# Kernel optimization log

Measured on AMD Instinct MI355X. Metric: run time of the kernel, lower is better.

Reference implementation:

```python
import jax, jax.numpy as jnp
import numpy as np

B, L, D = 4, 2048, 256
H, DH, MLP, MAX_REL = 8, 32, 1024, 16
LN_EPS = 1e-5


def _layernorm(x, g, b):
    mu = jnp.mean(x, axis=-1, keepdims=True)
    var = jnp.mean(jnp.square(x - mu), axis=-1, keepdims=True)
    return (x - mu) * jax.lax.rsqrt(var + LN_EPS) * g + b


def setup_inputs() -> dict:
    key = jax.random.key(0)
    ks = jax.random.split(key, 16)
    s = 0.02
    return {
        "x": jax.random.normal(ks[0], (B, L, D), jnp.float32),
        "key_padding_mask": jax.random.randint(ks[1], (B, L), 0, 2).astype(bool),
        "Wqkv": jax.random.normal(ks[2], (D, 3 * D), jnp.float32) * s,
        "bqkv": jnp.zeros((3 * D,), jnp.float32),
        "Wo": jax.random.normal(ks[3], (D, D), jnp.float32) * s,
        "bo": jnp.zeros((D,), jnp.float32),
        "ln1_g": jnp.ones((D,), jnp.float32),
        "ln1_b": jnp.zeros((D,), jnp.float32),
        "W1": jax.random.normal(ks[4], (D, MLP), jnp.float32) * s,
        "b1": jnp.zeros((MLP,), jnp.float32),
        "W2": jax.random.normal(ks[5], (MLP, D), jnp.float32) * s,
        "b2": jnp.zeros((D,), jnp.float32),
        "ln2_g": jnp.ones((D,), jnp.float32),
        "ln2_b": jnp.zeros((D,), jnp.float32),
        "rel_bias": jax.random.normal(ks[6], (2 * MAX_REL + 1, H), jnp.float32) * 0.01,
    }


def reference(x, key_padding_mask, Wqkv, bqkv, Wo, bo, ln1_g, ln1_b,
              W1, b1, W2, b2, ln2_g, ln2_b, rel_bias):
    Bx, Lw, Dm = x.shape
    scale = DH ** -0.5
    qkv = x @ Wqkv + bqkv                                   # [B,L,3D]
    q, k, v = jnp.split(qkv, 3, axis=-1)
    q = q.reshape(Bx, Lw, H, DH).transpose(0, 2, 1, 3)      # [B,H,L,dh]
    k = k.reshape(Bx, Lw, H, DH).transpose(0, 2, 1, 3)
    v = v.reshape(Bx, Lw, H, DH).transpose(0, 2, 1, 3)
    scores = jnp.einsum("bhqd,bhkd->bhqk", q, k) * scale    # [B,H,L,L]
    idx = jnp.arange(Lw)
    rel_clip = jnp.clip(idx[None, :] - idx[:, None], -MAX_REL, MAX_REL) + MAX_REL
    bias = rel_bias[rel_clip].transpose(2, 0, 1)            # [H,L,L]
    scores = scores + bias[None]
    scores = jnp.where(key_padding_mask[:, None, None, :], jnp.float32(-1e9), scores)
    attn = jax.nn.softmax(scores, axis=-1)                  # dropout = identity (eval)
    out = jnp.einsum("bhqk,bhkd->bhqd", attn, v)
    out = out.transpose(0, 2, 1, 3).reshape(Bx, Lw, Dm)
    out = out @ Wo + bo
    x = _layernorm(x + out, ln1_g, ln1_b)
    m = jax.nn.relu(x @ W1 + b1) @ W2 + b2
    x = _layernorm(x + m, ln2_g, ln2_b)
    return x
```

## Files before the change

kernel.cpp:

```cpp
#include <hip/hip_runtime.h>

#define B_   4
#define L_   2048
#define D_   256
#define H_   8
#define DH_  32
#define MLP_ 1024
#define LOG2E 1.4426950408889634f

typedef __attribute__((ext_vector_type(8))) short  short8;
typedef __attribute__((ext_vector_type(4))) float  f32x4;
typedef __attribute__((ext_vector_type(2))) float  f32x2;
typedef unsigned long long ull;

union FragU { short8 v; struct { ull lo, hi; } q; unsigned u[4]; };
union SU { f32x4 v4; f32x2 v2[2]; };

__device__ __forceinline__ unsigned short f2bf(float f) {
  unsigned u = __float_as_uint(f);
  u += 0x7fffu + ((u >> 16) & 1u);
  return (unsigned short)(u >> 16);
}

__device__ __forceinline__ ull pack4(float a, float b, float c, float d) {
  return (ull)f2bf(a) | ((ull)f2bf(b) << 16) | ((ull)f2bf(c) << 32) | ((ull)f2bf(d) << 48);
}

__device__ __forceinline__ unsigned cvt_pk_bf16(float lo, float hi) {
  unsigned r;
  asm("v_cvt_pk_bf16_f32 %0, %1, %2" : "=v"(r) : "v"(lo), "v"(hi));
  return r;
}

__device__ __forceinline__ f32x2 pk_add(f32x2 a, f32x2 b) {
  f32x2 r; asm("v_pk_add_f32 %0, %1, %2" : "=v"(r) : "v"(a), "v"(b)); return r;
}

__device__ __forceinline__ float fexp2(float x) {
#if __has_builtin(__builtin_amdgcn_exp2f)
  return __builtin_amdgcn_exp2f(x);
#else
  return exp2f(x);
#endif
}

#define GLL16(gp, lp) __builtin_amdgcn_global_load_lds( \
    (const __attribute__((address_space(1))) void*)(gp), \
    (__attribute__((address_space(3))) void*)(lp), 16, 0, 0)

__global__ void prep_w(const float* __restrict__ x,
                       const float* __restrict__ Wqkv, const float* __restrict__ Wo,
                       const float* __restrict__ W1, const float* __restrict__ W2,
                       const int* __restrict__ mask, const float* __restrict__ relb,
                       unsigned short* __restrict__ xb,
                       unsigned short* __restrict__ wqkvt, unsigned short* __restrict__ wot,
                       unsigned short* __restrict__ w1t, unsigned short* __restrict__ w2t,
                       float* __restrict__ maskf,
                       float* __restrict__ mlo, float* __restrict__ mhi) {
  const int i = blockIdx.x * 256 + threadIdx.x;
  if (i < 524288) {
    const float4 v = *(const float4*)(x + (size_t)i * 4);
    *(ull*)(xb + (size_t)i * 4) = pack4(v.x, v.y, v.z, v.w);
  } else if (i < 720896) {
    const int j = i - 524288, r = j / 768, c = j - r * 768;
    wqkvt[(size_t)c * 256 + r] = f2bf(Wqkv[j]);
  } else if (i < 786432) {
    const int j = i - 720896, r = j >> 8, c = j & 255;
    wot[(size_t)c * 256 + r] = f2bf(Wo[j]);
  } else if (i < 1048576) {
    const int j = i - 786432, r = j >> 10, c = j & 1023;
    w1t[(size_t)c * 256 + r] = f2bf(W1[j]);
  } else if (i < 1310720) {
    const int j = i - 1048576, r = j >> 8, c = j & 255;
    w2t[(size_t)c * 1024 + r] = f2bf(W2[j]);
  } else if (i < 1318912) {
    const int j = i - 1310720;
    maskf[j] = mask[j] ? -1e9f : 0.f;
  } else {
    const int j2 = i - 1318912;
    const int t = j2 >> 16, idx = j2 & 65535;
    const int bh = idx >> 11, j = idx & 2047;
    const int bq = bh >> 3, h = bh & 7;
    const float base = mask[bq * L_ + j] ? -1e9f : 0.f;
    const float bias = relb[(t ? 32 * H_ : 0) + h] * LOG2E;
    (t ? mhi : mlo)[idx] = base + bias;
  }
}

template <int MODE, int TM, int TN, int NBX, int BYG>
__launch_bounds__(256)
__global__ void gemm_k(const unsigned short* __restrict__ A,
                       const unsigned short* __restrict__ Bt,
                       const float* __restrict__ bias,
                       unsigned short* __restrict__ outb0,
                       unsigned short* __restrict__ outb1,
                       unsigned short* __restrict__ outb2,
                       int K)
{
  constexpr int MI = TM / 32, NI = TN / 32;
  __shared__ alignas(16) unsigned short As[2][TM * 64];
  __shared__ alignas(16) unsigned short Bs[2][TN * 64];
  const int tid  = threadIdx.x;
  const int lane = tid & 63, wv = tid >> 6;
  const int wr = wv >> 1, wc = wv & 1;
  const int lr = lane & 15, g = lane >> 4;
  const int bid = blockIdx.x;
  const int xcd = bid & 7, ii = bid >> 3;
  const int by = xcd * BYG + ii / NBX;
  const int bx = ii % NBX;
  const int m0 = by * TM, n0 = bx * TN;
  const int l8 = lane >> 3, jj = lane & 7;

  auto stage = [&](int buf, int k0) {
#pragma unroll
    for (int i = 0; i < MI; ++i) {
      const int row = i * 32 + wv * 8 + l8;
      GLL16(A + (size_t)(m0 + row) * K + k0 + ((jj ^ (row & 7)) * 8),
            &As[buf][i * 2048 + wv * 512]);
    }
#pragma unroll
    for (int i = 0; i < NI; ++i) {
      const int row = i * 32 + wv * 8 + l8;
      GLL16(Bt + (size_t)(n0 + row) * K + k0 + ((jj ^ (row & 7)) * 8),
            &Bs[buf][i * 2048 + wv * 512]);
    }
  };

  f32x4 acc[MI][NI];
#pragma unroll
  for (int i = 0; i < MI; ++i)
#pragma unroll
    for (int j = 0; j < NI; ++j) acc[i][j] = (f32x4)(0.f);

  stage(0, 0);
  for (int k0 = 0; k0 < K; k0 += 64) {
    const int cur = (k0 >> 6) & 1;
    if (k0 + 64 < K) {
      stage(cur ^ 1, k0 + 64);
      asm volatile("s_waitcnt vmcnt(%0)" :: "n"(MI + NI) : "memory");
    } else {
      asm volatile("s_waitcnt vmcnt(0)" ::: "memory");
    }
    __builtin_amdgcn_sched_barrier(0);
    __builtin_amdgcn_s_barrier();
#pragma unroll
    for (int kk = 0; kk < 2; ++kk) {
      FragU af[MI], bf[NI];
#pragma unroll
      for (int mi = 0; mi < MI; ++mi) {
        const int row = wr * (TM / 2) + mi * 16 + lr;
        const int sw = (row & 7) << 3;
        af[mi].q.lo = *(const ull*)&As[cur][row * 64 + ((kk * 32 + 4 * g) ^ sw)];
        af[mi].q.hi = *(const ull*)&As[cur][row * 64 + ((kk * 32 + 16 + 4 * g) ^ sw)];
      }
#pragma unroll
      for (int ni = 0; ni < NI; ++ni) {
        const int row = wc * (TN / 2) + ni * 16 + lr;
        const int sw = (row & 7) << 3;
        bf[ni].q.lo = *(const ull*)&Bs[cur][row * 64 + ((kk * 32 + 4 * g) ^ sw)];
        bf[ni].q.hi = *(const ull*)&Bs[cur][row * 64 + ((kk * 32 + 16 + 4 * g) ^ sw)];
      }
#pragma unroll
      for (int mi = 0; mi < MI; ++mi)
#pragma unroll
        for (int ni = 0; ni < NI; ++ni)
          acc[mi][ni] = __builtin_amdgcn_mfma_f32_16x16x32_bf16(af[mi].v, bf[ni].v, acc[mi][ni], 0, 0, 0);
    }
    asm volatile("s_waitcnt lgkmcnt(0)" ::: "memory");
    __builtin_amdgcn_sched_barrier(0);
    __builtin_amdgcn_s_barrier();
  }

#pragma unroll
  for (int mi = 0; mi < MI; ++mi) {
#pragma unroll
    for (int ni = 0; ni < NI; ++ni) {
      const int n = n0 + wc * (TN / 2) + ni * 16 + lr;
      const float bv = bias[n];
#pragma unroll
      for (int r = 0; r < 4; ++r) {
        const int m = m0 + wr * (TM / 2) + mi * 16 + 4 * g + r;
        float val = acc[mi][ni][r] + bv;
        if constexpr (MODE == 0) {
          const int s = n >> 8, hh = (n >> 5) & 7, dh = n & 31;
          const int bb = m >> 11, l = m & (L_ - 1);
          if (s == 0) {
            outb0[((size_t)(bb * H_ + hh) * L_ + l) * DH_ + dh] =
                f2bf(val * (0.17677669529663687f * LOG2E));
          } else if (s == 1) {
            outb1[((size_t)(bb * H_ + hh) * L_ + l) * DH_ + dh] = f2bf(val);
          } else {
            outb2[((size_t)(bb * H_ + hh) * DH_ + dh) * L_ + l] = f2bf(val);
          }
        } else {
          outb0[(size_t)m * MLP_ + n] = f2bf(fmaxf(val, 0.f));
        }
      }
    }
  }
}

template <bool WRITE_BF>
__launch_bounds__(512)
__global__ void gemmln_k(const unsigned short* __restrict__ A,
                         const unsigned short* __restrict__ Bt,
                         const float* __restrict__ bias,
                         const float* __restrict__ resid,
                         const float* __restrict__ lng,
                         const float* __restrict__ lnb,
                         float* __restrict__ outf,
                         unsigned short* __restrict__ outb,
                         int K)
{
  __shared__ alignas(16) unsigned short As[2][16 * 64];
  __shared__ alignas(16) unsigned short Bs[2][256 * 64];
  __shared__ float rsum[8][16], rsq[8][16], rmu[16], rrstd[16];
  const int tid  = threadIdx.x;
  const int lane = tid & 63, wv = tid >> 6;
  const int lr = lane & 15, g = lane >> 4;
  const int m0 = blockIdx.x * 16;
  const int l8 = lane >> 3, jj = lane & 7;

  auto stage = [&](int buf, int k0) {
    if (wv < 2) {
      const int row = wv * 8 + l8;
      GLL16(A + (size_t)(m0 + row) * K + k0 + ((jj ^ (row & 7)) * 8),
            &As[buf][wv * 512]);
    }
#pragma unroll
    for (int i = 0; i < 4; ++i) {
      const int n = i * 64 + wv * 8 + l8;
      GLL16(Bt + (size_t)n * K + k0 + ((jj ^ (n & 7)) * 8),
            &Bs[buf][i * 4096 + wv * 512]);
    }
  };

  f32x4 acc[2];
  acc[0] = (f32x4)(0.f); acc[1] = (f32x4)(0.f);

  stage(0, 0);
  for (int k0 = 0; k0 < K; k0 += 64) {
    const int cur = (k0 >> 6) & 1;
    if (k0 + 64 < K) {
      stage(cur ^ 1, k0 + 64);
      asm volatile("s_waitcnt vmcnt(4)" ::: "memory");
    } else {
      asm volatile("s_waitcnt vmcnt(0)" ::: "memory");
    }
    __builtin_amdgcn_sched_barrier(0);
    __builtin_amdgcn_s_barrier();
#pragma unroll
    for (int kk = 0; kk < 2; ++kk) {
      FragU af, bf[2];
      {
        const int sw = (lr & 7) << 3;
        af.q.lo = *(const ull*)&As[cur][lr * 64 + ((kk * 32 + 4 * g) ^ sw)];
        af.q.hi = *(const ull*)&As[cur][lr * 64 + ((kk * 32 + 16 + 4 * g) ^ sw)];
      }
#pragma unroll
      for (int ni = 0; ni < 2; ++ni) {
        const int row = wv * 32 + ni * 16 + lr;
        const int sw = (row & 7) << 3;
        bf[ni].q.lo = *(const ull*)&Bs[cur][row * 64 + ((kk * 32 + 4 * g) ^ sw)];
        bf[ni].q.hi = *(const ull*)&Bs[cur][row * 64 + ((kk * 32 + 16 + 4 * g) ^ sw)];
      }
#pragma unroll
      for (int ni = 0; ni < 2; ++ni)
        acc[ni] = __builtin_amdgcn_mfma_f32_16x16x32_bf16(af.v, bf[ni].v, acc[ni], 0, 0, 0);
    }
    asm volatile("s_waitcnt lgkmcnt(0)" ::: "memory");
    __builtin_amdgcn_sched_barrier(0);
    __builtin_amdgcn_s_barrier();
  }

  float g2[2], b2[2], bias2[2];
  int col[2];
#pragma unroll
  for (int ni = 0; ni < 2; ++ni) {
    col[ni] = wv * 32 + ni * 16 + lr;
    g2[ni] = lng[col[ni]]; b2[ni] = lnb[col[ni]]; bias2[ni] = bias[col[ni]];
  }
  float vals[2][4];
#pragma unroll
  for (int r = 0; r < 4; ++r) {
    const int row = 4 * g + r;
    float s = 0.f, q = 0.f;
#pragma unroll
    for (int ni = 0; ni < 2; ++ni) {
      float v = acc[ni][r] + bias2[ni] + resid[(size_t)(m0 + row) * D_ + col[ni]];
      vals[ni][r] = v; s += v; q += v * v;
    }
#pragma unroll
    for (int off = 1; off < 16; off <<= 1) {
      s += __shfl_xor(s, off); q += __shfl_xor(q, off);
    }
    if (lr == 0) { rsum[wv][row] = s; rsq[wv][row] = q; }
  }
  __syncthreads();
  if (tid < 16) {
    float s = 0.f, q = 0.f;
#pragma unroll
    for (int w = 0; w < 8; ++w) { s += rsum[w][tid]; q += rsq[w][tid]; }
    const float mu = s * (1.f / D_);
    rmu[tid] = mu;
    rrstd[tid] = rsqrtf(q * (1.f / D_) - mu * mu + 1e-5f);
  }
  __syncthreads();
#pragma unroll
  for (int r = 0; r < 4; ++r) {
    const int row = 4 * g + r;
    const float mu = rmu[row], rs = rrstd[row];
#pragma unroll
    for (int ni = 0; ni < 2; ++ni) {
      const float o = (vals[ni][r] - mu) * rs * g2[ni] + b2[ni];
      const size_t idx = (size_t)(m0 + row) * D_ + col[ni];
      outf[idx] = o;
      if constexpr (WRITE_BF) outb[idx] = f2bf(o);
    }
  }
}

__launch_bounds__(512)
__global__ void attn_k(const unsigned short* __restrict__ qb,
                       const unsigned short* __restrict__ kp,
                       const unsigned short* __restrict__ vT,
                       const float* __restrict__ maskf,
                       const float* __restrict__ mlo,
                       const float* __restrict__ mhi,
                       const float* __restrict__ relb,
                       unsigned short* __restrict__ aout)
{
  __shared__ alignas(16) unsigned short Ks[2][128 * 40];
  __shared__ alignas(16) unsigned short Vs[2][32 * 128];
  __shared__ alignas(16) float biasv[36];
  const int tid = threadIdx.x;
  const int lane = tid & 63, wv = tid >> 6;
  const int lr = lane & 15, g = lane >> 4;
  const int bid = blockIdx.x;
  const int ii = bid >> 3;
  const int bh = (bid & 7) * 4 + (ii >> 4);
  const int qblk = ii & 15;
  const int b = bh >> 3, h = bh & 7;
  const size_t bhoff = (size_t)bh * (L_ * DH_);
  if (tid < 33) biasv[tid] = relb[tid * H_ + h] * LOG2E;
  const int qw0 = qblk * 128 + wv * 16;

  FragU qf;
  {
    const unsigned short* qr = qb + bhoff + (size_t)(qw0 + lr) * DH_;
    qf.q.lo = *(const ull*)(qr + 4 * g);
    qf.q.hi = *(const ull*)(qr + 16 + 4 * g);
  }
  f32x4 O0 = (f32x4)(0.f), O1 = (f32x4)(0.f);
  f32x2 ssum2 = {0.f, 0.f};
  const f32x4 z4 = (f32x4)(0.f);
  const int krow = tid >> 2, koff = (tid & 3) * 8;
  const float* mtl = mlo + (size_t)bh * L_ + 4 * g;
  const float* mth = mhi + (size_t)bh * L_ + 4 * g;
  const float* mbn = maskf + (size_t)b * L_ + 4 * g;

  {
    const int4 ka = *(const int4*)(kp + bhoff + (size_t)krow * DH_ + koff);
    const int d = wv * 4 + (lane >> 4);
    GLL16(vT + ((size_t)bh * DH_ + d) * L_ + (((lane & 15) * 8) ^ ((d & 7) * 8)),
          &Vs[0][wv * 512]);
    *(int4*)&Ks[0][krow * 40 + koff] = ka;
    asm volatile("s_waitcnt vmcnt(0) lgkmcnt(0)" ::: "memory");
    __builtin_amdgcn_s_barrier();
  }

#pragma unroll 2
  for (int ch = 0; ch < 16; ++ch) {
    const int cur = ch & 1, nxt = cur ^ 1;
    const int kv = ch * 128;
    const bool more = ch < 15;
    int4 ka = {0, 0, 0, 0};
    if (more) {
      ka = *(const int4*)(kp + bhoff + (size_t)(kv + 128 + krow) * DH_ + koff);
      const int d = wv * 4 + (lane >> 4);
      GLL16(vT + ((size_t)bh * DH_ + d) * L_ + kv + 128 + (((lane & 15) * 8) ^ ((d & 7) * 8)),
            &Vs[nxt][wv * 512]);
    }

    SU sT[2][4];
#pragma unroll
    for (int st = 0; st < 2; ++st) {
      const unsigned short* KsC = &Ks[cur][st * 64 * 40];
#pragma unroll
      for (int jt = 0; jt < 4; ++jt) {
        FragU kf;
        const int base = (jt * 16 + lr) * 40;
        kf.q.lo = *(const ull*)&KsC[base + 4 * g];
        kf.q.hi = *(const ull*)&KsC[base + 16 + 4 * g];
        sT[st][jt].v4 = __builtin_amdgcn_mfma_f32_16x16x32_bf16(kf.v, qf.v, z4, 0, 0, 0);
      }
    }

#pragma unroll
    for (int st = 0; st < 2; ++st) {
      const int j0 = kv + st * 64;
      const int dlt = j0 - qw0;
      if (dlt >= 32 || dlt <= -80) {
        const float* mt = (dlt > 0) ? mth : mtl;
#pragma unroll
        for (int jt = 0; jt < 4; ++jt) {
          SU mk; mk.v4 = *(const f32x4*)(mt + j0 + jt * 16);
          sT[st][jt].v2[0] = pk_add(sT[st][jt].v2[0], mk.v2[0]);
          sT[st][jt].v2[1] = pk_add(sT[st][jt].v2[1], mk.v2[1]);
        }
      } else {
#pragma unroll
        for (int jt = 0; jt < 4; ++jt)
#pragma unroll
          for (int r = 0; r < 4; ++r) {
            int rel = j0 + jt * 16 + 4 * g + r - (qw0 + lr);
            rel = rel < -16 ? -16 : (rel > 16 ? 16 : rel);
            sT[st][jt].v4[r] += biasv[rel + 16] + mbn[j0 + jt * 16 + r];
          }
      }
#pragma unroll
      for (int jt = 0; jt < 4; ++jt)
#pragma unroll
        for (int r = 0; r < 4; ++r)
          sT[st][jt].v4[r] = fexp2(sT[st][jt].v4[r]);
      const f32x2 s01 = pk_add(sT[st][0].v2[0], sT[st][0].v2[1]);
      const f32x2 s23 = pk_add(sT[st][1].v2[0], sT[st][1].v2[1]);
      const f32x2 s45 = pk_add(sT[st][2].v2[0], sT[st][2].v2[1]);
      const f32x2 s67 = pk_add(sT[st][3].v2[0], sT[st][3].v2[1]);
      ssum2 = pk_add(ssum2, pk_add(pk_add(s01, s23), pk_add(s45, s67)));

      FragU a0, a1;
      a0.u[0] = cvt_pk_bf16(sT[st][0].v4[0], sT[st][0].v4[1]);
      a0.u[1] = cvt_pk_bf16(sT[st][0].v4[2], sT[st][0].v4[3]);
      a0.u[2] = cvt_pk_bf16(sT[st][1].v4[0], sT[st][1].v4[1]);
      a0.u[3] = cvt_pk_bf16(sT[st][1].v4[2], sT[st][1].v4[3]);
      a1.u[0] = cvt_pk_bf16(sT[st][2].v4[0], sT[st][2].v4[1]);
      a1.u[1] = cvt_pk_bf16(sT[st][2].v4[2], sT[st][2].v4[3]);
      a1.u[2] = cvt_pk_bf16(sT[st][3].v4[0], sT[st][3].v4[1]);
      a1.u[3] = cvt_pk_bf16(sT[st][3].v4[2], sT[st][3].v4[3]);

      FragU vf00, vf01, vf10, vf11;
#pragma unroll
      for (int dt = 0; dt < 2; ++dt) {
        const int row = dt * 16 + lr;
        const int sw = (row & 7) << 3;
        FragU v0, v1;
        v0.q.lo = *(const ull*)&Vs[cur][row * 128 + ((st * 64 + 4 * g) ^ sw)];
        v0.q.hi = *(const ull*)&Vs[cur][row * 128 + ((st * 64 + 16 + 4 * g) ^ sw)];
        v1.q.lo = *(const ull*)&Vs[cur][row * 128 + ((st * 64 + 32 + 4 * g) ^ sw)];
        v1.q.hi = *(const ull*)&Vs[cur][row * 128 + ((st * 64 + 48 + 4 * g) ^ sw)];
        if (dt == 0) { vf00 = v0; vf01 = v1; } else { vf10 = v0; vf11 = v1; }
      }
      O0 = __builtin_amdgcn_mfma_f32_16x16x32_bf16(a0.v, vf00.v, O0, 0, 0, 0);
      O0 = __builtin_amdgcn_mfma_f32_16x16x32_bf16(a1.v, vf01.v, O0, 0, 0, 0);
      O1 = __builtin_amdgcn_mfma_f32_16x16x32_bf16(a0.v, vf10.v, O1, 0, 0, 0);
      O1 = __builtin_amdgcn_mfma_f32_16x16x32_bf16(a1.v, vf11.v, O1, 0, 0, 0);
    }

    if (more) {
      *(int4*)&Ks[nxt][krow * 40 + koff] = ka;
    }
    asm volatile("s_waitcnt vmcnt(0) lgkmcnt(0)" ::: "memory");
    __builtin_amdgcn_sched_barrier(0);
    __builtin_amdgcn_s_barrier();
  }

  float ssum = ssum2[0] + ssum2[1];
  ssum += __shfl_xor(ssum, 16);
  ssum += __shfl_xor(ssum, 32);
#pragma unroll
  for (int r = 0; r < 4; ++r) {
    const float sden = __shfl(ssum, 4 * g + r);
    const float inv = 1.f / sden;
    const int qo = qw0 + 4 * g + r;
    unsigned short* orow = aout + ((size_t)(b * L_ + qo)) * D_ + h * DH_;
    orow[lr]      = f2bf(O0[r] * inv);
    orow[16 + lr] = f2bf(O1[r] * inv);
  }
}

extern "C" void kernel_launch(void* const* d_in, const int* in_sizes, int n_in,
                              void* d_out, int out_size, void* d_ws, size_t ws_size,
                              hipStream_t stream) {
  (void)in_sizes; (void)n_in; (void)out_size; (void)ws_size;
  const float* x    = (const float*)d_in[0];
  const int*   mask = (const int*)d_in[1];
  const float* Wqkv = (const float*)d_in[2];
  const float* bqkv = (const float*)d_in[3];
  const float* Wo   = (const float*)d_in[4];
  const float* bo   = (const float*)d_in[5];
  const float* ln1g = (const float*)d_in[6];
  const float* ln1b = (const float*)d_in[7];
  const float* W1   = (const float*)d_in[8];
  const float* b1   = (const float*)d_in[9];
  const float* W2   = (const float*)d_in[10];
  const float* b2   = (const float*)d_in[11];
  const float* ln2g = (const float*)d_in[12];
  const float* ln2b = (const float*)d_in[13];
  const float* relb = (const float*)d_in[14];

  size_t off = 0;
  char* wsb = (char*)d_ws;
  auto carve = [&](size_t bytes) -> void* {
    void* p = wsb + off;
    off += (bytes + 255) & ~(size_t)255;
    return p;
  };
  const size_t tokb = (size_t)B_ * L_;
  unsigned short* xb    = (unsigned short*)carve(tokb * D_ * 2);
  unsigned short* qbuf  = (unsigned short*)carve(tokb * D_ * 2);
  unsigned short* kbuf  = (unsigned short*)carve(tokb * D_ * 2);
  unsigned short* vTb   = (unsigned short*)carve(tokb * D_ * 2);
  unsigned short* attnb = (unsigned short*)carve(tokb * D_ * 2);
  unsigned short* wqkvt = (unsigned short*)carve((size_t)3 * D_ * D_ * 2);
  unsigned short* wot   = (unsigned short*)carve((size_t)D_ * D_ * 2);
  unsigned short* w1t   = (unsigned short*)carve((size_t)D_ * MLP_ * 2);
  unsigned short* w2t   = (unsigned short*)carve((size_t)D_ * MLP_ * 2);
  float*          x1    = (float*)carve(tokb * D_ * 4);
  unsigned short* x1b   = (unsigned short*)carve(tokb * D_ * 2);
  unsigned short* hbuf  = (unsigned short*)carve(tokb * MLP_ * 2);
  float*          maskfb = (float*)carve(tokb * 4);
  float*          mlob  = (float*)carve((size_t)B_ * H_ * L_ * 4);
  float*          mhib  = (float*)carve((size_t)B_ * H_ * L_ * 4);

  prep_w<<<5664, 256, 0, stream>>>(x, Wqkv, Wo, W1, W2, mask, relb,
                                   xb, wqkvt, wot, w1t, w2t, maskfb, mlob, mhib);

  gemm_k<0, 64, 128, 6, 16><<<768, 256, 0, stream>>>(
      xb, wqkvt, bqkv, qbuf, kbuf, vTb, D_);
  attn_k<<<512, 512, 0, stream>>>(
      qbuf, kbuf, vTb, maskfb, mlob, mhib, relb, attnb);
  gemmln_k<true><<<tokb / 16, 512, 0, stream>>>(
      attnb, wot, bo, x, ln1g, ln1b, x1, x1b, D_);
  gemm_k<2, 64, 128, 8, 16><<<1024, 256, 0, stream>>>(
      x1b, w1t, b1, hbuf, nullptr, nullptr, D_);
  gemmln_k<false><<<tokb / 16, 512, 0, stream>>>(
      hbuf, w2t, b2, x1, ln2g, ln2b, (float*)d_out, nullptr, MLP_);
}
```

Measured before the change: 111.5 us.

## Load K fragments directly to registers in attention; tile weight transposes via LDS

```diff
diff --git a/kernel.cpp b/kernel.cpp
--- a/kernel.cpp
+++ b/kernel.cpp
@@ -49,41 +49,51 @@
     (__attribute__((address_space(3))) void*)(lp), 16, 0, 0)
 
 __global__ void prep_w(const float* __restrict__ x,
-                       const float* __restrict__ Wqkv, const float* __restrict__ Wo,
-                       const float* __restrict__ W1, const float* __restrict__ W2,
                        const int* __restrict__ mask, const float* __restrict__ relb,
                        unsigned short* __restrict__ xb,
-                       unsigned short* __restrict__ wqkvt, unsigned short* __restrict__ wot,
-                       unsigned short* __restrict__ w1t, unsigned short* __restrict__ w2t,
                        float* __restrict__ maskf,
                        float* __restrict__ mlo, float* __restrict__ mhi) {
   const int i = blockIdx.x * 256 + threadIdx.x;
   if (i < 524288) {
     const float4 v = *(const float4*)(x + (size_t)i * 4);
     *(ull*)(xb + (size_t)i * 4) = pack4(v.x, v.y, v.z, v.w);
-  } else if (i < 720896) {
-    const int j = i - 524288, r = j / 768, c = j - r * 768;
-    wqkvt[(size_t)c * 256 + r] = f2bf(Wqkv[j]);
-  } else if (i < 786432) {
-    const int j = i - 720896, r = j >> 8, c = j & 255;
-    wot[(size_t)c * 256 + r] = f2bf(Wo[j]);
-  } else if (i < 1048576) {
-    const int j = i - 786432, r = j >> 10, c = j & 1023;
-    w1t[(size_t)c * 256 + r] = f2bf(W1[j]);
-  } else if (i < 1310720) {
-    const int j = i - 1048576, r = j >> 8, c = j & 255;
-    w2t[(size_t)c * 1024 + r] = f2bf(W2[j]);
-  } else if (i < 1318912) {
-    const int j = i - 1310720;
+  } else if (i < 532480) {
+    const int j = i - 524288;
     maskf[j] = mask[j] ? -1e9f : 0.f;
   } else {
-    const int j2 = i - 1318912;
+    const int j2 = i - 532480;
     const int t = j2 >> 16, idx = j2 & 65535;
     const int bh = idx >> 11, j = idx & 2047;
     const int bq = bh >> 3, h = bh & 7;
     const float base = mask[bq * L_ + j] ? -1e9f : 0.f;
     const float bias = relb[(t ? 32 * H_ : 0) + h] * LOG2E;
     (t ? mhi : mlo)[idx] = base + bias;
+  }
+}
+
+__launch_bounds__(256)
+__global__ void prep_t(const float* __restrict__ Wqkv, const float* __restrict__ Wo,
+                       const float* __restrict__ W1, const float* __restrict__ W2,
+                       unsigned short* __restrict__ wqkvt, unsigned short* __restrict__ wot,
+                       unsigned short* __restrict__ w1t, unsigned short* __restrict__ w2t) {
+  __shared__ float tile[32][33];
+  const int bid = blockIdx.x;
+  const float* src; unsigned short* dst; int R, C, tr, tc;
+  if (bid < 192)      { src = Wqkv; dst = wqkvt; R = 256;  C = 768;  tr = bid / 24;          tc = bid % 24; }
+  else if (bid < 256) { src = Wo;   dst = wot;   R = 256;  C = 256;  tr = (bid - 192) >> 3;  tc = (bid - 192) & 7; }
+  else if (bid < 512) { src = W1;   dst = w1t;   R = 256;  C = 1024; tr = (bid - 256) >> 5;  tc = (bid - 256) & 31; }
+  else                { src = W2;   dst = w2t;   R = 1024; C = 256;  tr = (bid - 512) >> 3;  tc = (bid - 512) & 7; }
+  const int tx = threadIdx.x & 31, ty = threadIdx.x >> 5;
+#pragma unroll
+  for (int i = 0; i < 4; ++i) {
+    const int r = tr * 32 + ty + i * 8;
+    tile[ty + i * 8][tx] = src[(size_t)r * C + tc * 32 + tx];
+  }
+  __syncthreads();
+#pragma unroll
+  for (int i = 0; i < 4; ++i) {
+    const int c = tc * 32 + ty + i * 8;
+    dst[(size_t)c * R + tr * 32 + tx] = f2bf(tile[tx][ty + i * 8]);
   }
 }
 
@@ -330,7 +340,6 @@
                        const float* __restrict__ relb,
                        unsigned short* __restrict__ aout)
 {
-  __shared__ alignas(16) unsigned short Ks[2][128 * 40];
   __shared__ alignas(16) unsigned short Vs[2][32 * 128];
   __shared__ alignas(16) float biasv[36];
   const int tid = threadIdx.x;
@@ -346,25 +355,26 @@
   const int qw0 = qblk * 128 + wv * 16;
 
   FragU qf;
-  {
-    const unsigned short* qr = qb + bhoff + (size_t)(qw0 + lr) * DH_;
-    qf.q.lo = *(const ull*)(qr + 4 * g);
-    qf.q.hi = *(const ull*)(qr + 16 + 4 * g);
-  }
+  qf.v = *(const short8*)(qb + bhoff + (size_t)(qw0 + lr) * DH_ + 8 * g);
+
   f32x4 O0 = (f32x4)(0.f), O1 = (f32x4)(0.f);
   f32x2 ssum2 = {0.f, 0.f};
   const f32x4 z4 = (f32x4)(0.f);
-  const int krow = tid >> 2, koff = (tid & 3) * 8;
+  const unsigned short* kb0 = kp + bhoff + (size_t)lr * DH_ + 8 * g;
   const float* mtl = mlo + (size_t)bh * L_ + 4 * g;
   const float* mth = mhi + (size_t)bh * L_ + 4 * g;
   const float* mbn = maskf + (size_t)b * L_ + 4 * g;
 
+  FragU kreg[8];
+#pragma unroll
+  for (int st = 0; st < 2; ++st)
+#pragma unroll
+    for (int jt = 0; jt < 4; ++jt)
+      kreg[st * 4 + jt].v = *(const short8*)(kb0 + (size_t)(st * 64 + jt * 16) * DH_);
   {
-    const int4 ka = *(const int4*)(kp + bhoff + (size_t)krow * DH_ + koff);
     const int d = wv * 4 + (lane >> 4);
     GLL16(vT + ((size_t)bh * DH_ + d) * L_ + (((lane & 15) * 8) ^ ((d & 7) * 8)),
           &Vs[0][wv * 512]);
-    *(int4*)&Ks[0][krow * 40 + koff] = ka;
     asm volatile("s_waitcnt vmcnt(0) lgkmcnt(0)" ::: "memory");
     __builtin_amdgcn_s_barrier();
   }
@@ -374,9 +384,7 @@
     const int cur = ch & 1, nxt = cur ^ 1;
     const int kv = ch * 128;
     const bool more = ch < 15;
-    int4 ka = {0, 0, 0, 0};
     if (more) {
-      ka = *(const int4*)(kp + bhoff + (size_t)(kv + 128 + krow) * DH_ + koff);
       const int d = wv * 4 + (lane >> 4);
       GLL16(vT + ((size_t)bh * DH_ + d) * L_ + kv + 128 + (((lane & 15) * 8) ^ ((d & 7) * 8)),
             &Vs[nxt][wv * 512]);
@@ -384,16 +392,18 @@
 
     SU sT[2][4];
 #pragma unroll
-    for (int st = 0; st < 2; ++st) {
-      const unsigned short* KsC = &Ks[cur][st * 64 * 40];
-#pragma unroll
-      for (int jt = 0; jt < 4; ++jt) {
-        FragU kf;
-        const int base = (jt * 16 + lr) * 40;
-        kf.q.lo = *(const ull*)&KsC[base + 4 * g];
-        kf.q.hi = *(const ull*)&KsC[base + 16 + 4 * g];
-        sT[st][jt].v4 = __builtin_amdgcn_mfma_f32_16x16x32_bf16(kf.v, qf.v, z4, 0, 0, 0);
-      }
+    for (int st = 0; st < 2; ++st)
+#pragma unroll
+      for (int jt = 0; jt < 4; ++jt)
+        sT[st][jt].v4 = __builtin_amdgcn_mfma_f32_16x16x32_bf16(kreg[st * 4 + jt].v, qf.v, z4, 0, 0, 0);
+
+    if (more) {
+#pragma unroll
+      for (int st = 0; st < 2; ++st)
+#pragma unroll
+        for (int jt = 0; jt < 4; ++jt)
+          kreg[st * 4 + jt].v =
+              *(const short8*)(kb0 + (size_t)(kv + 128 + st * 64 + jt * 16) * DH_);
     }
 
 #pragma unroll
@@ -458,11 +468,10 @@
     }
 
     if (more) {
-      *(int4*)&Ks[nxt][krow * 40 + koff] = ka;
-    }
-    asm volatile("s_waitcnt vmcnt(0) lgkmcnt(0)" ::: "memory");
-    __builtin_amdgcn_sched_barrier(0);
-    __builtin_amdgcn_s_barrier();
+      asm volatile("s_waitcnt vmcnt(8) lgkmcnt(0)" ::: "memory");
+      __builtin_amdgcn_sched_barrier(0);
+      __builtin_amdgcn_s_barrier();
+    }
   }
 
   float ssum = ssum2[0] + ssum2[1];
@@ -523,8 +532,8 @@
   float*          mlob  = (float*)carve((size_t)B_ * H_ * L_ * 4);
   float*          mhib  = (float*)carve((size_t)B_ * H_ * L_ * 4);
 
-  prep_w<<<5664, 256, 0, stream>>>(x, Wqkv, Wo, W1, W2, mask, relb,
-                                   xb, wqkvt, wot, w1t, w2t, maskfb, mlob, mhib);
+  prep_w<<<2592, 256, 0, stream>>>(x, mask, relb, xb, maskfb, mlob, mhib);
+  prep_t<<<768, 256, 0, stream>>>(Wqkv, Wo, W1, W2, wqkvt, wot, w1t, w2t);
 
   gemm_k<0, 64, 128, 6, 16><<<768, 256, 0, stream>>>(
       xb, wqkvt, bqkv, qbuf, kbuf, vTb, D_);
```

After: 126.4 us. 1.13x slower.
